# Optimization experiments

Hardware: AMD Instinct MI355X
Metric: run time of the kernel (lower is better)

The kernel has to match this reference:

```python
import jax, jax.numpy as jnp
import numpy as np

DIM = 256
HEADS = 4
DEPTH = DIM // HEADS
EXPAND = 4
EPS = 1e-3  # keras BatchNormalization default epsilon


def _bn(x, gamma, beta, mean, var):
    # inference-mode batch norm over last axis
    return gamma * (x - mean) * jax.lax.rsqrt(var + EPS) + beta


def setup_inputs() -> dict:
    key = jax.random.key(0)
    ks = jax.random.split(key, 12)
    B, S, D = 4, 2048, DIM
    H = D * EXPAND
    s = 1.0 / np.sqrt(D)
    inp = {
        "x": jax.random.normal(ks[0], (B, S, D), jnp.float32),
        "bn1_gamma": jnp.ones((D,), jnp.float32),
        "bn1_beta": jnp.zeros((D,), jnp.float32),
        "bn1_mean": jax.random.normal(ks[1], (D,), jnp.float32) * 0.1,
        "bn1_var": jnp.abs(jax.random.normal(ks[2], (D,), jnp.float32)) + 0.5,
        "wq": jax.random.normal(ks[3], (D, D), jnp.float32) * s,
        "bq": jnp.zeros((D,), jnp.float32),
        "wk": jax.random.normal(ks[4], (D, D), jnp.float32) * s,
        "bk": jnp.zeros((D,), jnp.float32),
        "wv": jax.random.normal(ks[5], (D, D), jnp.float32) * s,
        "bv": jnp.zeros((D,), jnp.float32),
        "wo": jax.random.normal(ks[6], (D, D), jnp.float32) * s,
        "bo": jnp.zeros((D,), jnp.float32),
        "bn2_gamma": jnp.ones((D,), jnp.float32),
        "bn2_beta": jnp.zeros((D,), jnp.float32),
        "bn2_mean": jax.random.normal(ks[7], (D,), jnp.float32) * 0.1,
        "bn2_var": jnp.abs(jax.random.normal(ks[8], (D,), jnp.float32)) + 0.5,
        "w1": jax.random.normal(ks[9], (D, H), jnp.float32) * s,
        "w2": jax.random.normal(ks[10], (H, D), jnp.float32) * (1.0 / np.sqrt(H)),
    }
    return inp


def reference(x, bn1_gamma, bn1_beta, bn1_mean, bn1_var,
              wq, bq, wk, bk, wv, bv, wo, bo,
              bn2_gamma, bn2_beta, bn2_mean, bn2_var, w1, w2):
    B, S, D = x.shape
    h = _bn(x, bn1_gamma, bn1_beta, bn1_mean, bn1_var)
    # project and split heads -> [B, H, S, depth]
    def heads(t):
        return t.reshape(B, S, HEADS, DEPTH).transpose(0, 2, 1, 3)
    q = heads(h @ wq + bq)
    k = heads(h @ wk + bk)
    v = heads(h @ wv + bv)
    scores = jnp.einsum("bhqd,bhkd->bhqk", q, k) / jnp.sqrt(jnp.float32(DEPTH))
    attn = jax.nn.softmax(scores, axis=-1)
    ctx = jnp.einsum("bhqk,bhkd->bhqd", attn, v)
    ctx = ctx.transpose(0, 2, 1, 3).reshape(B, S, D)
    attn_out = ctx @ wo + bo
    x1 = attn_out + x  # residual (dropout = identity at inference)
    h2 = _bn(x1, bn2_gamma, bn2_beta, bn2_mean, bn2_var)
    m = jax.nn.gelu(h2 @ w1, approximate=False) @ w2
    return m + x1
```

## Files before the change

kernel.cpp:

```cpp
#include <hip/hip_runtime.h>

typedef unsigned short u16;
typedef unsigned int u32;
typedef short short8 __attribute__((ext_vector_type(8)));
typedef short short4v __attribute__((ext_vector_type(4)));
typedef float f32x4 __attribute__((ext_vector_type(4)));

#define EPS 1e-3f
#define C1F 0.18033688011112042f

#if defined(__HIP_DEVICE_COMPILE__)
#define MFMA16(a, b, c) __builtin_amdgcn_mfma_f32_16x16x16bf16_1k(a, b, c, 0, 0, 0)
#else
#define MFMA16(a, b, c) (c)
#endif

static __device__ __forceinline__ u16 f2bf(float f) {
    u32 u = __float_as_uint(f);
    u += 0x7fffu + ((u >> 16) & 1u);
    return (u16)(u >> 16);
}
static __device__ __forceinline__ float bf2f(u16 v) {
    u32 u = (u32)v << 16;
    return __uint_as_float(u);
}
static __device__ __forceinline__ u32 pack_bf2(float a, float b) {
    u32 ua = __float_as_uint(a) + 0x8000u;
    u32 ub = __float_as_uint(b) + 0x8000u;
    return __builtin_amdgcn_perm(ub, ua, 0x07060302u);
}
static __device__ __forceinline__ void async_cp16(const void* g, void* l) {
    __builtin_amdgcn_global_load_lds(
        (const __attribute__((address_space(1))) unsigned int*)g,
        (__attribute__((address_space(3))) unsigned int*)l, 16, 0, 0);
}

__global__ void prep_kernel(const float* __restrict__ wq, const float* __restrict__ wk,
                            const float* __restrict__ wv, const float* __restrict__ wo,
                            const float* __restrict__ w1, const float* __restrict__ w2,
                            const float* __restrict__ bq, const float* __restrict__ bk,
                            const float* __restrict__ bv,
                            const float* __restrict__ g1, const float* __restrict__ b1,
                            const float* __restrict__ m1, const float* __restrict__ v1,
                            const float* __restrict__ g2, const float* __restrict__ b2,
                            const float* __restrict__ m2, const float* __restrict__ v2,
                            u16* __restrict__ wqkvT, u16* __restrict__ woT,
                            u16* __restrict__ w1T, u16* __restrict__ w2T,
                            float* __restrict__ bqkv,
                            float* __restrict__ bn1sc, float* __restrict__ bn1sh,
                            float* __restrict__ bn2sc, float* __restrict__ bn2sh) {
    int idx = blockIdx.x * 256 + threadIdx.x;
    if (idx < 196608) {
        int n = idx >> 8, k = idx & 255;
        float v;
        if (n < 256)      v = wq[k * 256 + n];
        else if (n < 512) v = wk[k * 256 + (n - 256)] * C1F;
        else              v = wv[k * 256 + (n - 512)];
        wqkvT[idx] = f2bf(v);
    } else if (idx < 262144) {
        int i = idx - 196608; int n = i >> 8, k = i & 255;
        woT[i] = f2bf(wo[k * 256 + n]);
    } else if (idx < 524288) {
        int i = idx - 262144; int n = i >> 8, k = i & 255;
        w1T[i] = f2bf(w1[k * 1024 + n]);
    } else if (idx < 786432) {
        int i = idx - 524288; int n = i >> 10, k = i & 1023;
        w2T[i] = f2bf(w2[k * 256 + n]);
    } else if (idx < 787200) {
        int i = idx - 786432;
        bqkv[i] = (i < 256) ? bq[i] : (i < 512 ? bk[i - 256] * C1F : bv[i - 512]);
    } else if (idx < 787456) {
        int i = idx - 787200;
        float sc = g1[i] * rsqrtf(v1[i] + EPS);
        bn1sc[i] = sc; bn1sh[i] = b1[i] - m1[i] * sc;
    } else if (idx < 787712) {
        int i = idx - 787456;
        float sc = g2[i] * rsqrtf(v2[i] + EPS);
        bn2sc[i] = sc; bn2sh[i] = b2[i] - m2[i] * sc;
    }
}

__global__ void bn1_kernel(const float* __restrict__ x, const float* __restrict__ sc,
                           const float* __restrict__ sh, u16* __restrict__ h) {
    int idx = blockIdx.x * 256 + threadIdx.x;
    int base = idx * 4;
    int c = base & 255;
    float4 xv = *(const float4*)(x + base);
    float4 s4 = *(const float4*)(sc + c);
    float4 h4 = *(const float4*)(sh + c);
    ushort4 pk;
    pk.x = f2bf(fmaf(xv.x, s4.x, h4.x));
    pk.y = f2bf(fmaf(xv.y, s4.y, h4.y));
    pk.z = f2bf(fmaf(xv.z, s4.z, h4.z));
    pk.w = f2bf(fmaf(xv.w, s4.w, h4.w));
    *(ushort4*)(h + base) = pk;
}

template <int EPI, int MT>
__global__ __launch_bounds__(256) void gemm_sd(
        const u16* __restrict__ A, const u16* __restrict__ Bt,
        int M, int N, int K,
        const float* __restrict__ bias, const float* __restrict__ resid,
        float* __restrict__ out_f32, u16* __restrict__ out_bf,
        u16* __restrict__ out_vt,
        const float* __restrict__ b2sc, const float* __restrict__ b2sh) {
    __shared__ u16 abuf[MT * 32 * 64];
    __shared__ u16 bbuf[128 * 64];
    const int t = threadIdx.x;
    const int w = t >> 6, lane = t & 63;
    const int l = lane & 15, Q = lane >> 4;
    const int m0 = blockIdx.x * (MT * 32);
    const int n0 = blockIdx.y * 128;
    const int rowh = (w & 1) * (MT * 16);
    const int colh = (w >> 1) * 64;

    f32x4 acc[MT][4];
#pragma unroll
    for (int mt = 0; mt < MT; ++mt)
#pragma unroll
        for (int nt = 0; nt < 4; ++nt) acc[mt][nt] = (f32x4){0.f, 0.f, 0.f, 0.f};

    for (int k0 = 0; k0 < K; k0 += 64) {
        __syncthreads();
#pragma unroll
        for (int j = 0; j < MT; ++j) {
            int idx = j * 256 + t;
            int r = idx >> 3, c8 = idx & 7;
            int sc = c8 ^ (r & 7);
            async_cp16(A + (size_t)(m0 + r) * K + k0 + sc * 8, abuf + idx * 8);
        }
#pragma unroll
        for (int j = 0; j < 4; ++j) {
            int idx = j * 256 + t;
            int r = idx >> 3, c8 = idx & 7;
            int sc = c8 ^ (r & 7);
            async_cp16(Bt + (size_t)(n0 + r) * K + k0 + sc * 8, bbuf + idx * 8);
        }
        __syncthreads();
#pragma unroll
        for (int kd = 0; kd < 2; ++kd) {
            short8 bfr[4];
#pragma unroll
            for (int nt = 0; nt < 4; ++nt) {
                int r = colh + nt * 16 + l;
                int slot = (kd * 4 + Q) ^ (r & 7);
                bfr[nt] = *(const short8*)(bbuf + r * 64 + slot * 8);
            }
#pragma unroll
            for (int mt = 0; mt < MT; ++mt) {
                int r = rowh + mt * 16 + l;
                int slot = (kd * 4 + Q) ^ (r & 7);
                short8 afr = *(const short8*)(abuf + r * 64 + slot * 8);
#pragma unroll
                for (int nt = 0; nt < 4; ++nt)
                    acc[mt][nt] = __builtin_amdgcn_mfma_f32_16x16x32_bf16(afr, bfr[nt], acc[mt][nt], 0, 0, 0);
            }
        }
    }

#pragma unroll
    for (int mt = 0; mt < MT; ++mt)
#pragma unroll
        for (int nt = 0; nt < 4; ++nt) {
            int col = n0 + colh + nt * 16 + l;
            int row0 = m0 + rowh + mt * 16 + Q * 4;
            if (EPI == 0) {
                float b = bias[col];
                if (col < 512) {
#pragma unroll
                    for (int r = 0; r < 4; ++r)
                        out_bf[(size_t)(row0 + r) * 512 + col] = f2bf(acc[mt][nt][r] + b);
                } else {
                    ushort4 pk;
                    pk.x = f2bf(acc[mt][nt][0] + b);
                    pk.y = f2bf(acc[mt][nt][1] + b);
                    pk.z = f2bf(acc[mt][nt][2] + b);
                    pk.w = f2bf(acc[mt][nt][3] + b);
                    *(ushort4*)(out_vt + (size_t)(col - 512) * 8192 + row0) = pk;
                }
            } else {
#pragma unroll
                for (int r = 0; r < 4; ++r) {
                    int row = row0 + r;
                    float val = acc[mt][nt][r];
                    size_t oidx = (size_t)row * N + col;
                    if (EPI == 1) {
                        val += bias[col] + resid[oidx];
                        out_f32[oidx] = val;
                        out_bf[oidx] = f2bf(fmaf(val, b2sc[col], b2sh[col]));
                    } else if (EPI == 2) {
                        float gl = 0.5f * val * (1.f + erff(val * 0.70710678118654752f));
                        out_bf[oidx] = f2bf(gl);
                    } else {
                        out_f32[oidx] = val + resid[oidx];
                    }
                }
            }
        }
}

static __device__ __forceinline__ void stage_tiles(const u16* kglob, const u16* vglob,
                                                   u16* kdst, u16* vdst,
                                                   int w, int lane, int kt) {
#pragma unroll
    for (int j = 0; j < 2; ++j) {
        int cw = (w * 2 + j) * 64 + lane;
        int r = cw >> 3;
        int c = (cw & 7) ^ (r & 7);
        async_cp16(kglob + ((size_t)(kt * 64 + r)) * 512 + c * 8, kdst + (w * 2 + j) * 512);
        async_cp16(vglob + ((size_t)r) * 8192 + kt * 64 + c * 8, vdst + (w * 2 + j) * 512);
    }
}

__global__ __launch_bounds__(256) void attn_kernel(const u16* __restrict__ qk,
                                                   const u16* __restrict__ vT,
                                                   u16* __restrict__ opart,
                                                   float* __restrict__ lpart) {
    __shared__ u16 kbuf[2][4096];
    __shared__ u16 vbuf[2][4096];
    const int t = threadIdx.x;
    const int w = t >> 6, lane = t & 63;
    const int l = lane & 15, Q = lane >> 4;
    const int qt = blockIdx.x;
    const int bh = blockIdx.y;
    const int sp = blockIdx.z;
    const int bb = bh >> 2, hd = bh & 3;
    const size_t rowbase = (size_t)bb * 2048;
    const int q0 = qt * 128 + w * 32;

    short8 qf[2][2];
#pragma unroll
    for (int qg = 0; qg < 2; ++qg)
#pragma unroll
        for (int kd = 0; kd < 2; ++kd)
            qf[qg][kd] = *(const short8*)(qk + (rowbase + q0 + qg * 16 + l) * 512
                                          + hd * 64 + kd * 32 + Q * 8);

    f32x4 o[2][4];
#pragma unroll
    for (int qg = 0; qg < 2; ++qg)
#pragma unroll
        for (int dt = 0; dt < 4; ++dt) o[qg][dt] = (f32x4){0.f, 0.f, 0.f, 0.f};
    float lacc[2] = {0.f, 0.f};

    const u16* kglob = qk + (rowbase + sp * 512) * 512 + 256 + hd * 64;
    const u16* vglob = vT + ((size_t)(hd * 64)) * 8192 + rowbase + sp * 512;

    stage_tiles(kglob, vglob, kbuf[0], vbuf[0], w, lane, 0);

    for (int kt = 0; kt < 8; ++kt) {
        __syncthreads();
        if (kt < 7)
            stage_tiles(kglob, vglob, kbuf[(kt + 1) & 1], vbuf[(kt + 1) & 1], w, lane, kt + 1);
        const u16* kb = kbuf[kt & 1];
        const u16* vb = vbuf[kt & 1];

        union { u32 u[2]; short4v s4; } pf[2][4];
#pragma unroll
        for (int st = 0; st < 4; ++st) {
            int r = st * 16 + l;
            short8 kf0 = *(const short8*)(kb + r * 64 + ((Q) ^ (r & 7)) * 8);
            short8 kf1 = *(const short8*)(kb + r * 64 + ((4 + Q) ^ (r & 7)) * 8);
#pragma unroll
            for (int qg = 0; qg < 2; ++qg) {
                f32x4 s = (f32x4){0.f, 0.f, 0.f, 0.f};
                s = __builtin_amdgcn_mfma_f32_16x16x32_bf16(kf0, qf[qg][0], s, 0, 0, 0);
                s = __builtin_amdgcn_mfma_f32_16x16x32_bf16(kf1, qf[qg][1], s, 0, 0, 0);
                float p0 = exp2f(fminf(s[0], 100.f));
                float p1 = exp2f(fminf(s[1], 100.f));
                float p2 = exp2f(fminf(s[2], 100.f));
                float p3 = exp2f(fminf(s[3], 100.f));
                lacc[qg] += (p0 + p1) + (p2 + p3);
                pf[qg][st].u[0] = pack_bf2(p0, p1);
                pf[qg][st].u[1] = pack_bf2(p2, p3);
            }
        }

#pragma unroll
        for (int c = 0; c < 4; ++c) {
#pragma unroll
            for (int dt = 0; dt < 4; ++dt) {
                int r = dt * 16 + l;
                int slot = (2 * c + (Q >> 1)) ^ (r & 7);
                short4v vf = *(const short4v*)(vb + r * 64 + slot * 8 + (Q & 1) * 4);
                o[0][dt] = MFMA16(vf, pf[0][c].s4, o[0][dt]);
                o[1][dt] = MFMA16(vf, pf[1][c].s4, o[1][dt]);
            }
        }
    }

#pragma unroll
    for (int qg = 0; qg < 2; ++qg) {
        float v = lacc[qg];
        v += __shfl_xor(v, 16);
        v += __shfl_xor(v, 32);
        lacc[qg] = v;
    }
    u16* ob = opart + (((size_t)sp * 16 + bh) * 2048 + q0) * 64;
#pragma unroll
    for (int qg = 0; qg < 2; ++qg)
#pragma unroll
        for (int dt = 0; dt < 4; ++dt) {
            ushort4 pk;
            pk.x = f2bf(o[qg][dt][0]);
            pk.y = f2bf(o[qg][dt][1]);
            pk.z = f2bf(o[qg][dt][2]);
            pk.w = f2bf(o[qg][dt][3]);
            *(ushort4*)(ob + (size_t)(qg * 16 + l) * 64 + dt * 16 + Q * 4) = pk;
        }
    if (Q == 0) {
        size_t lb = ((size_t)sp * 16 + bh) * 2048 + q0;
        lpart[lb + l] = lacc[0];
        lpart[lb + 16 + l] = lacc[1];
    }
}

__global__ void combine_kernel(const u16* __restrict__ opart,
                               const float* __restrict__ lpart,
                               u16* __restrict__ ctx) {
    int idx = blockIdx.x * 256 + threadIdx.x;
    int e = idx * 4;
    int row = e >> 8, col = e & 255;
    int b = row >> 11, s = row & 2047, h = col >> 6, d = col & 63;
    float a0 = 0.f, a1 = 0.f, a2 = 0.f, a3 = 0.f, lsum = 0.f;
#pragma unroll
    for (int sp = 0; sp < 4; ++sp) {
        size_t pb = (((size_t)sp * 16 + b * 4 + h) * 2048 + s) * 64 + d;
        ushort4 ov = *(const ushort4*)(opart + pb);
        a0 += bf2f(ov.x); a1 += bf2f(ov.y); a2 += bf2f(ov.z); a3 += bf2f(ov.w);
        lsum += lpart[((size_t)sp * 16 + b * 4 + h) * 2048 + s];
    }
    float li = 1.0f / lsum;
    ushort4 pk;
    pk.x = f2bf(a0 * li);
    pk.y = f2bf(a1 * li);
    pk.z = f2bf(a2 * li);
    pk.w = f2bf(a3 * li);
    *(ushort4*)(ctx + e) = pk;
}

extern "C" void kernel_launch(void* const* d_in, const int* in_sizes, int n_in,
                              void* d_out, int out_size, void* d_ws, size_t ws_size,
                              hipStream_t stream) {
    (void)in_sizes; (void)n_in; (void)out_size; (void)ws_size;
    const float* x  = (const float*)d_in[0];
    const float* g1 = (const float*)d_in[1];
    const float* b1 = (const float*)d_in[2];
    const float* m1 = (const float*)d_in[3];
    const float* v1 = (const float*)d_in[4];
    const float* wq = (const float*)d_in[5];
    const float* bq = (const float*)d_in[6];
    const float* wk = (const float*)d_in[7];
    const float* bk = (const float*)d_in[8];
    const float* wv = (const float*)d_in[9];
    const float* bv = (const float*)d_in[10];
    const float* wo = (const float*)d_in[11];
    const float* bo = (const float*)d_in[12];
    const float* g2 = (const float*)d_in[13];
    const float* b2 = (const float*)d_in[14];
    const float* m2 = (const float*)d_in[15];
    const float* v2 = (const float*)d_in[16];
    const float* w1 = (const float*)d_in[17];
    const float* w2 = (const float*)d_in[18];

    char* ws = (char*)d_ws;
    u16*   qkb    = (u16*)(ws + 0);
    u16*   ctxh   = (u16*)(ws + 8388608);
    float* x1     = (float*)(ws + 12582912);
    float* lpart  = (float*)(ws + 12582912);
    u16*   h2     = (u16*)(ws + 20971520);
    u16*   opart  = (u16*)(ws + 25165824);
    u16*   gbuf   = (u16*)(ws + 25165824);
    u16*   vTb    = (u16*)(ws + 41943040);
    u16*   wqkvT  = (u16*)(ws + 46137344);
    u16*   woT    = (u16*)(ws + 46530560);
    u16*   w1T    = (u16*)(ws + 46661632);
    u16*   w2T    = (u16*)(ws + 47185920);
    float* bqkv   = (float*)(ws + 47710208);
    float* bn1sc  = (float*)(ws + 47713280);
    float* bn1sh  = (float*)(ws + 47714304);
    float* bn2sc  = (float*)(ws + 47715328);
    float* bn2sh  = (float*)(ws + 47716352);
    u16*   h_buf  = ctxh;
    u16*   ctx    = ctxh;
    float* out    = (float*)d_out;

    prep_kernel<<<3077, 256, 0, stream>>>(wq, wk, wv, wo, w1, w2, bq, bk, bv,
                                          g1, b1, m1, v1, g2, b2, m2, v2,
                                          wqkvT, woT, w1T, w2T, bqkv,
                                          bn1sc, bn1sh, bn2sc, bn2sh);
    bn1_kernel<<<2048, 256, 0, stream>>>(x, bn1sc, bn1sh, h_buf);
    gemm_sd<0, 4><<<dim3(64, 6), 256, 0, stream>>>(
        h_buf, wqkvT, 8192, 768, 256, bqkv, nullptr, nullptr, qkb, vTb, nullptr, nullptr);
    attn_kernel<<<dim3(16, 16, 4), 256, 0, stream>>>(qkb, vTb, opart, lpart);
    combine_kernel<<<2048, 256, 0, stream>>>(opart, lpart, ctx);
    gemm_sd<1, 2><<<dim3(128, 2), 256, 0, stream>>>(
        ctx, woT, 8192, 256, 256, bo, x, x1, h2, nullptr, bn2sc, bn2sh);
    gemm_sd<2, 4><<<dim3(64, 8), 256, 0, stream>>>(
        h2, w1T, 8192, 1024, 256, nullptr, nullptr, nullptr, gbuf, nullptr, nullptr, nullptr);
    gemm_sd<3, 2><<<dim3(128, 2), 256, 0, stream>>>(
        gbuf, w2T, 8192, 256, 1024, nullptr, x1, out, nullptr, nullptr, nullptr, nullptr);
}
```

Measured before the change: 196.4 us.

## Shrink GEMM tiles to 64x64 and double attention key splits

Replaces the 128-wide GEMM tiles with 64x64 tiles, so every GEMM launches far more workgroups. The attention split-K count goes from 4 to 8 and its LDS double buffering is dropped in favour of a single buffer, with the combine kernel now summing 8 partials. The workspace layout is reorganized to hold the larger partial buffers. The aim is more parallelism to fill the MI355X compute units, at the cost of less data reuse per tile, lost load/compute overlap, and more partial-output traffic.

```diff
diff --git a/kernel.cpp b/kernel.cpp
--- a/kernel.cpp
+++ b/kernel.cpp
@@ -96,41 +96,36 @@
     *(ushort4*)(h + base) = pk;
 }
 
-template <int EPI, int MT>
-__global__ __launch_bounds__(256) void gemm_sd(
+template <int EPI>
+__global__ __launch_bounds__(256) void gemm64(
         const u16* __restrict__ A, const u16* __restrict__ Bt,
         int M, int N, int K,
         const float* __restrict__ bias, const float* __restrict__ resid,
         float* __restrict__ out_f32, u16* __restrict__ out_bf,
         u16* __restrict__ out_vt,
         const float* __restrict__ b2sc, const float* __restrict__ b2sh) {
-    __shared__ u16 abuf[MT * 32 * 64];
-    __shared__ u16 bbuf[128 * 64];
+    __shared__ u16 abuf[64 * 64];
+    __shared__ u16 bbuf[64 * 64];
     const int t = threadIdx.x;
     const int w = t >> 6, lane = t & 63;
     const int l = lane & 15, Q = lane >> 4;
-    const int m0 = blockIdx.x * (MT * 32);
-    const int n0 = blockIdx.y * 128;
-    const int rowh = (w & 1) * (MT * 16);
-    const int colh = (w >> 1) * 64;
-
-    f32x4 acc[MT][4];
-#pragma unroll
-    for (int mt = 0; mt < MT; ++mt)
-#pragma unroll
-        for (int nt = 0; nt < 4; ++nt) acc[mt][nt] = (f32x4){0.f, 0.f, 0.f, 0.f};
+    const int m0 = blockIdx.x * 64;
+    const int n0 = blockIdx.y * 64;
+
+    f32x4 acc[4];
+#pragma unroll
+    for (int nt = 0; nt < 4; ++nt) acc[nt] = (f32x4){0.f, 0.f, 0.f, 0.f};
 
     for (int k0 = 0; k0 < K; k0 += 64) {
-        __syncthreads();
-#pragma unroll
-        for (int j = 0; j < MT; ++j) {
+#pragma unroll
+        for (int j = 0; j < 2; ++j) {
             int idx = j * 256 + t;
             int r = idx >> 3, c8 = idx & 7;
             int sc = c8 ^ (r & 7);
             async_cp16(A + (size_t)(m0 + r) * K + k0 + sc * 8, abuf + idx * 8);
         }
 #pragma unroll
-        for (int j = 0; j < 4; ++j) {
+        for (int j = 0; j < 2; ++j) {
             int idx = j * 256 + t;
             int r = idx >> 3, c8 = idx & 7;
             int sc = c8 ^ (r & 7);
@@ -139,64 +134,55 @@
         __syncthreads();
 #pragma unroll
         for (int kd = 0; kd < 2; ++kd) {
-            short8 bfr[4];
+            int ar = w * 16 + l;
+            short8 afr = *(const short8*)(abuf + ar * 64 + (((kd * 4 + Q) ^ (ar & 7))) * 8);
 #pragma unroll
             for (int nt = 0; nt < 4; ++nt) {
-                int r = colh + nt * 16 + l;
-                int slot = (kd * 4 + Q) ^ (r & 7);
-                bfr[nt] = *(const short8*)(bbuf + r * 64 + slot * 8);
-            }
-#pragma unroll
-            for (int mt = 0; mt < MT; ++mt) {
-                int r = rowh + mt * 16 + l;
-                int slot = (kd * 4 + Q) ^ (r & 7);
-                short8 afr = *(const short8*)(abuf + r * 64 + slot * 8);
-#pragma unroll
-                for (int nt = 0; nt < 4; ++nt)
-                    acc[mt][nt] = __builtin_amdgcn_mfma_f32_16x16x32_bf16(afr, bfr[nt], acc[mt][nt], 0, 0, 0);
-            }
-        }
-    }
-
-#pragma unroll
-    for (int mt = 0; mt < MT; ++mt)
-#pragma unroll
-        for (int nt = 0; nt < 4; ++nt) {
-            int col = n0 + colh + nt * 16 + l;
-            int row0 = m0 + rowh + mt * 16 + Q * 4;
-            if (EPI == 0) {
-                float b = bias[col];
-                if (col < 512) {
-#pragma unroll
-                    for (int r = 0; r < 4; ++r)
-                        out_bf[(size_t)(row0 + r) * 512 + col] = f2bf(acc[mt][nt][r] + b);
+                int r = nt * 16 + l;
+                short8 bfr = *(const short8*)(bbuf + r * 64 + (((kd * 4 + Q) ^ (r & 7))) * 8);
+                acc[nt] = __builtin_amdgcn_mfma_f32_16x16x32_bf16(afr, bfr, acc[nt], 0, 0, 0);
+            }
+        }
+        __syncthreads();
+    }
+
+#pragma unroll
+    for (int nt = 0; nt < 4; ++nt) {
+        int col = n0 + nt * 16 + l;
+        int row0 = m0 + w * 16 + Q * 4;
+        if (EPI == 0) {
+            float b = bias[col];
+            if (col < 512) {
+#pragma unroll
+                for (int r = 0; r < 4; ++r)
+                    out_bf[(size_t)(row0 + r) * 512 + col] = f2bf(acc[nt][r] + b);
+            } else {
+                ushort4 pk;
+                pk.x = f2bf(acc[nt][0] + b);
+                pk.y = f2bf(acc[nt][1] + b);
+                pk.z = f2bf(acc[nt][2] + b);
+                pk.w = f2bf(acc[nt][3] + b);
+                *(ushort4*)(out_vt + (size_t)(col - 512) * 8192 + row0) = pk;
+            }
+        } else {
+#pragma unroll
+            for (int r = 0; r < 4; ++r) {
+                int row = row0 + r;
+                float val = acc[nt][r];
+                size_t oidx = (size_t)row * N + col;
+                if (EPI == 1) {
+                    val += bias[col] + resid[oidx];
+                    out_f32[oidx] = val;
+                    out_bf[oidx] = f2bf(fmaf(val, b2sc[col], b2sh[col]));
+                } else if (EPI == 2) {
+                    float gl = 0.5f * val * (1.f + erff(val * 0.70710678118654752f));
+                    out_bf[oidx] = f2bf(gl);
                 } else {
-                    ushort4 pk;
-                    pk.x = f2bf(acc[mt][nt][0] + b);
-                    pk.y = f2bf(acc[mt][nt][1] + b);
-                    pk.z = f2bf(acc[mt][nt][2] + b);
-                    pk.w = f2bf(acc[mt][nt][3] + b);
-                    *(ushort4*)(out_vt + (size_t)(col - 512) * 8192 + row0) = pk;
+                    out_f32[oidx] = val + resid[oidx];
                 }
-            } else {
-#pragma unroll
-                for (int r = 0; r < 4; ++r) {
-                    int row = row0 + r;
-                    float val = acc[mt][nt][r];
-                    size_t oidx = (size_t)row * N + col;
-                    if (EPI == 1) {
-                        val += bias[col] + resid[oidx];
-                        out_f32[oidx] = val;
-                        out_bf[oidx] = f2bf(fmaf(val, b2sc[col], b2sh[col]));
-                    } else if (EPI == 2) {
-                        float gl = 0.5f * val * (1.f + erff(val * 0.70710678118654752f));
-                        out_bf[oidx] = f2bf(gl);
-                    } else {
-                        out_f32[oidx] = val + resid[oidx];
-                    }
-                }
-            }
-        }
+            }
+        }
+    }
 }
 
 static __device__ __forceinline__ void stage_tiles(const u16* kglob, const u16* vglob,
@@ -216,8 +202,8 @@
                                                    const u16* __restrict__ vT,
                                                    u16* __restrict__ opart,
                                                    float* __restrict__ lpart) {
-    __shared__ u16 kbuf[2][4096];
-    __shared__ u16 vbuf[2][4096];
+    __shared__ u16 kbuf[4096];
+    __shared__ u16 vbuf[4096];
     const int t = threadIdx.x;
     const int w = t >> 6, lane = t & 63;
     const int l = lane & 15, Q = lane >> 4;
@@ -243,24 +229,19 @@
         for (int dt = 0; dt < 4; ++dt) o[qg][dt] = (f32x4){0.f, 0.f, 0.f, 0.f};
     float lacc[2] = {0.f, 0.f};
 
-    const u16* kglob = qk + (rowbase + sp * 512) * 512 + 256 + hd * 64;
-    const u16* vglob = vT + ((size_t)(hd * 64)) * 8192 + rowbase + sp * 512;
-
-    stage_tiles(kglob, vglob, kbuf[0], vbuf[0], w, lane, 0);
-
-    for (int kt = 0; kt < 8; ++kt) {
+    const u16* kglob = qk + (rowbase + sp * 256) * 512 + 256 + hd * 64;
+    const u16* vglob = vT + ((size_t)(hd * 64)) * 8192 + rowbase + sp * 256;
+
+    for (int kt = 0; kt < 4; ++kt) {
+        stage_tiles(kglob, vglob, kbuf, vbuf, w, lane, kt);
         __syncthreads();
-        if (kt < 7)
-            stage_tiles(kglob, vglob, kbuf[(kt + 1) & 1], vbuf[(kt + 1) & 1], w, lane, kt + 1);
-        const u16* kb = kbuf[kt & 1];
-        const u16* vb = vbuf[kt & 1];
 
         union { u32 u[2]; short4v s4; } pf[2][4];
 #pragma unroll
         for (int st = 0; st < 4; ++st) {
             int r = st * 16 + l;
-            short8 kf0 = *(const short8*)(kb + r * 64 + ((Q) ^ (r & 7)) * 8);
-            short8 kf1 = *(const short8*)(kb + r * 64 + ((4 + Q) ^ (r & 7)) * 8);
+            short8 kf0 = *(const short8*)(kbuf + r * 64 + ((Q) ^ (r & 7)) * 8);
+            short8 kf1 = *(const short8*)(kbuf + r * 64 + ((4 + Q) ^ (r & 7)) * 8);
 #pragma unroll
             for (int qg = 0; qg < 2; ++qg) {
                 f32x4 s = (f32x4){0.f, 0.f, 0.f, 0.f};
@@ -282,11 +263,12 @@
             for (int dt = 0; dt < 4; ++dt) {
                 int r = dt * 16 + l;
                 int slot = (2 * c + (Q >> 1)) ^ (r & 7);
-                short4v vf = *(const short4v*)(vb + r * 64 + slot * 8 + (Q & 1) * 4);
+                short4v vf = *(const short4v*)(vbuf + r * 64 + slot * 8 + (Q & 1) * 4);
                 o[0][dt] = MFMA16(vf, pf[0][c].s4, o[0][dt]);
                 o[1][dt] = MFMA16(vf, pf[1][c].s4, o[1][dt]);
             }
         }
+        __syncthreads();
     }
 
 #pragma unroll
@@ -324,7 +306,7 @@
     int b = row >> 11, s = row & 2047, h = col >> 6, d = col & 63;
     float a0 = 0.f, a1 = 0.f, a2 = 0.f, a3 = 0.f, lsum = 0.f;
 #pragma unroll
-    for (int sp = 0; sp < 4; ++sp) {
+    for (int sp = 0; sp < 8; ++sp) {
         size_t pb = (((size_t)sp * 16 + b * 4 + h) * 2048 + s) * 64 + d;
         ushort4 ov = *(const ushort4*)(opart + pb);
         a0 += bf2f(ov.x); a1 += bf2f(ov.y); a2 += bf2f(ov.z); a3 += bf2f(ov.w);
@@ -364,25 +346,24 @@
     const float* w2 = (const float*)d_in[18];
 
     char* ws = (char*)d_ws;
-    u16*   qkb    = (u16*)(ws + 0);
-    u16*   ctxh   = (u16*)(ws + 8388608);
-    float* x1     = (float*)(ws + 12582912);
-    float* lpart  = (float*)(ws + 12582912);
-    u16*   h2     = (u16*)(ws + 20971520);
-    u16*   opart  = (u16*)(ws + 25165824);
-    u16*   gbuf   = (u16*)(ws + 25165824);
-    u16*   vTb    = (u16*)(ws + 41943040);
-    u16*   wqkvT  = (u16*)(ws + 46137344);
-    u16*   woT    = (u16*)(ws + 46530560);
-    u16*   w1T    = (u16*)(ws + 46661632);
-    u16*   w2T    = (u16*)(ws + 47185920);
-    float* bqkv   = (float*)(ws + 47710208);
-    float* bn1sc  = (float*)(ws + 47713280);
-    float* bn1sh  = (float*)(ws + 47714304);
-    float* bn2sc  = (float*)(ws + 47715328);
-    float* bn2sh  = (float*)(ws + 47716352);
-    u16*   h_buf  = ctxh;
-    u16*   ctx    = ctxh;
+    u16*   qkb    = (u16*)(ws + (0ull << 20));
+    u16*   vTb    = (u16*)(ws + (8ull << 20));
+    u16*   h_buf  = (u16*)(ws + (12ull << 20));
+    u16*   ctx    = (u16*)(ws + (16ull << 20));
+    float* x1     = (float*)(ws + (20ull << 20));
+    u16*   h2     = (u16*)(ws + (28ull << 20));
+    u16*   gbuf   = (u16*)(ws + (32ull << 20));
+    u16*   opart  = (u16*)(ws + (48ull << 20));
+    float* lpart  = (float*)(ws + (80ull << 20));
+    u16*   wqkvT  = (u16*)(ws + (81ull << 20));
+    u16*   woT    = (u16*)(ws + (82ull << 20));
+    u16*   w1T    = (u16*)(ws + (83ull << 20));
+    u16*   w2T    = (u16*)(ws + (84ull << 20));
+    float* bqkv   = (float*)(ws + (85ull << 20));
+    float* bn1sc  = (float*)(ws + (85ull << 20) + 4096);
+    float* bn1sh  = (float*)(ws + (85ull << 20) + 8192);
+    float* bn2sc  = (float*)(ws + (85ull << 20) + 12288);
+    float* bn2sh  = (float*)(ws + (85ull << 20) + 16384);
     float* out    = (float*)d_out;
 
     prep_kernel<<<3077, 256, 0, stream>>>(wq, wk, wv, wo, w1, w2, bq, bk, bv,
@@ -390,14 +371,14 @@
                                           wqkvT, woT, w1T, w2T, bqkv,
                                           bn1sc, bn1sh, bn2sc, bn2sh);
     bn1_kernel<<<2048, 256, 0, stream>>>(x, bn1sc, bn1sh, h_buf);
-    gemm_sd<0, 4><<<dim3(64, 6), 256, 0, stream>>>(
+    gemm64<0><<<dim3(128, 12), 256, 0, stream>>>(
         h_buf, wqkvT, 8192, 768, 256, bqkv, nullptr, nullptr, qkb, vTb, nullptr, nullptr);
-    attn_kernel<<<dim3(16, 16, 4), 256, 0, stream>>>(qkb, vTb, opart, lpart);
+    attn_kernel<<<dim3(16, 16, 8), 256, 0, stream>>>(qkb, vTb, opart, lpart);
     combine_kernel<<<2048, 256, 0, stream>>>(opart, lpart, ctx);
-    gemm_sd<1, 2><<<dim3(128, 2), 256, 0, stream>>>(
+    gemm64<1><<<dim3(128, 4), 256, 0, stream>>>(
         ctx, woT, 8192, 256, 256, bo, x, x1, h2, nullptr, bn2sc, bn2sh);
-    gemm_sd<2, 4><<<dim3(64, 8), 256, 0, stream>>>(
+    gemm64<2><<<dim3(128, 16), 256, 0, stream>>>(
         h2, w1T, 8192, 1024, 256, nullptr, nullptr, nullptr, gbuf, nullptr, nullptr, nullptr);
-    gemm_sd<3, 2><<<dim3(128, 2), 256, 0, stream>>>(
+    gemm64<3><<<dim3(128, 4), 256, 0, stream>>>(
         gbuf, w2T, 8192, 256, 1024, nullptr, x1, out, nullptr, nullptr, nullptr, nullptr);
 }
```

Result: no change. 193.2 us (-1.6%).
